# Kernel tuning notes

Hardware: AMD Instinct MI355X
Metric: run time of the kernel (lower is better)

Reference implementation:

```python
import jax, jax.numpy as jnp
import numpy as np

EPS = 1e-5


def _layer_norm(x, w, b):
    mu = jnp.mean(x, axis=-1, keepdims=True)
    var = jnp.mean(jnp.square(x - mu), axis=-1, keepdims=True)
    return (x - mu) * jax.lax.rsqrt(var + EPS) * w + b


def setup_inputs() -> dict:
    key = jax.random.key(0)
    ks = jax.random.split(key, 8)
    b, n, d, h = 1, 512, 128, 128
    edges = jax.random.normal(ks[0], (b, n, n, d), dtype=jnp.float32)
    mask = jax.random.bernoulli(ks[1], 0.9, (b, n, n))  # True = valid
    s = 0.02
    return {
        "edges": edges,
        "mask": mask,
        "ln1_w": jnp.ones((d,), jnp.float32),
        "ln1_b": jnp.zeros((d,), jnp.float32),
        "W_fg": jax.random.normal(ks[2], (4 * h, d), jnp.float32) * s,
        "b_fg": jnp.zeros((4 * h,), jnp.float32),
        "W_go": jax.random.normal(ks[3], (d, d), jnp.float32) * s,
        "b_go": jnp.zeros((d,), jnp.float32),
        "ln2_w": jnp.ones((h,), jnp.float32),
        "ln2_b": jnp.zeros((h,), jnp.float32),
        "W_out": jax.random.normal(ks[4], (d, h), jnp.float32) * s,
        "b_out": jnp.zeros((d,), jnp.float32),
    }


def reference(edges, mask, ln1_w, ln1_b, W_fg, b_fg, W_go, b_go, ln2_w, ln2_b, W_out, b_out):
    h = W_fg.shape[0] // 4
    x = _layer_norm(edges, ln1_w, ln1_b)                         # [b,n,n,d]
    fg = jnp.einsum('bijd,ed->bije', x, W_fg) + b_fg             # [b,n,n,4h]
    feats, gates = fg[..., :2 * h], fg[..., 2 * h:]
    gated = feats * jax.nn.sigmoid(gates)                        # [b,n,n,2h]
    to_feats, from_feats = gated[..., :h], gated[..., h:]
    out_gate = jax.nn.sigmoid(jnp.einsum('bijd,ed->bije', x, W_go) + b_go)
    m = mask[..., None]                                          # True = keep
    to_feats = jnp.where(m, to_feats, 0.0)
    from_feats = jnp.where(m, from_feats, 0.0)
    out_gate = jnp.where(m, out_gate, 0.0)
    # triangle outgoing: contract over shared k axis per channel d
    tri = jnp.einsum('bikd,bjkd->bijd', to_feats, from_feats)    # [b,n,n,h]
    out = jnp.einsum('bijh,dh->bijd', _layer_norm(tri, ln2_w, ln2_b), W_out) + b_out
    return out_gate * out
```

## Files before the change

kernel.cpp:

```cpp
#include <hip/hip_runtime.h>

#define NSEQ 512
#define DCH 128
#define RTOT (NSEQ * NSEQ)

typedef __attribute__((ext_vector_type(8))) short bf16x8;
typedef __attribute__((ext_vector_type(4))) float f32x4;

__device__ __forceinline__ unsigned short f2bf(float v) {
  union { float f; unsigned int u; } x; x.f = v;
  unsigned int u = x.u;
  return (unsigned short)((u + 0x7fffu + ((u >> 16) & 1u)) >> 16);
}
__device__ __forceinline__ float bf2f(unsigned short s) {
  union { unsigned int u; float f; } x; x.u = ((unsigned int)s) << 16;
  return x.f;
}
__device__ __forceinline__ float sigmoidf(float x) { return 1.f / (1.f + __expf(-x)); }

__device__ __forceinline__ void async16(const unsigned short* g, unsigned short* l) {
  __builtin_amdgcn_global_load_lds(
      (const __attribute__((address_space(1))) unsigned int*)g,
      (__attribute__((address_space(3))) unsigned int*)l, 16, 0, 0);
}

__global__ void prep_kernel(const float* __restrict__ W_fg, const float* __restrict__ b_fg,
                            const float* __restrict__ W_go, const float* __restrict__ b_go,
                            const float* __restrict__ W_out,
                            unsigned short* __restrict__ Wc, float* __restrict__ bc,
                            unsigned short* __restrict__ Woutb) {
  int idx = blockIdx.x * 256 + threadIdx.x;
  if (idx < 640 * 128) {
    int rr = idx >> 7, k = idx & 127;
    float v, bv;
    if (rr < 512) {
      int m = rr >> 7;
      int srow = (m == 1) ? rr + 128 : (m == 2) ? rr - 128 : rr;
      v = W_fg[srow * 128 + k];
      bv = b_fg[srow];
    } else {
      int srow = rr - 512;
      v = W_go[srow * 128 + k];
      bv = b_go[srow];
    }
    Wc[idx] = f2bf(v);
    if (k == 0) bc[rr] = bv;
  } else {
    int i2 = idx - 640 * 128;
    if (i2 < 128 * 128) Woutb[i2] = f2bf(W_out[i2]);
  }
}

__global__ __launch_bounds__(256) void ln1_kernel(const float* __restrict__ edges,
                                                  const float* __restrict__ w,
                                                  const float* __restrict__ b,
                                                  unsigned short* __restrict__ xb) {
  int wv = threadIdx.x >> 6;
  int lane = threadIdx.x & 63;
  size_t row = (size_t)blockIdx.x * 4 + wv;
  const float2* e = (const float2*)(edges + row * 128);
  float2 v = e[lane];
  float s = v.x + v.y, sq = v.x * v.x + v.y * v.y;
#pragma unroll
  for (int off = 32; off; off >>= 1) {
    s += __shfl_xor(s, off);
    sq += __shfl_xor(sq, off);
  }
  float mu = s * (1.f / 128.f);
  float var = sq * (1.f / 128.f) - mu * mu;
  float rs = rsqrtf(var + 1e-5f);
  int c = lane * 2;
  float x0 = (v.x - mu) * rs * w[c] + b[c];
  float x1 = (v.y - mu) * rs * w[c + 1] + b[c + 1];
  unsigned int packed = (unsigned int)f2bf(x0) | ((unsigned int)f2bf(x1) << 16);
  ((unsigned int*)(xb + row * 128))[lane] = packed;
}

__global__ __launch_bounds__(256) void fg_gemm_kernel(
    const unsigned short* __restrict__ xb, const unsigned short* __restrict__ Wc,
    const float* __restrict__ bc, const int* __restrict__ mask,
    unsigned short* __restrict__ toT, unsigned short* __restrict__ fromT) {
  __shared__ unsigned int Cs[128 * 36];
  int nb = blockIdx.y;
  int wv = threadIdx.x >> 6, lane = threadIdx.x & 63;
  int qm = lane & 15, quad = lane >> 4;
  int r0 = blockIdx.x * 64;
  int nbase = nb * 256;

  bf16x8 Bf[2][4], Bg[2][4];
#pragma unroll
  for (int ft = 0; ft < 2; ft++)
#pragma unroll
    for (int kk = 0; kk < 4; kk++) {
      int ko = kk * 32 + quad * 8;
      Bf[ft][kk] = *(const bf16x8*)(Wc + (size_t)(nbase + wv * 32 + ft * 16 + qm) * 128 + ko);
      Bg[ft][kk] = *(const bf16x8*)(Wc + (size_t)(nbase + 128 + wv * 32 + ft * 16 + qm) * 128 + ko);
    }

#pragma unroll
  for (int m = 0; m < 4; m++) {
    int rw = r0 + m * 16;
    f32x4 accf[2], accg[2];
#pragma unroll
    for (int ft = 0; ft < 2; ft++) {
      accf[ft] = (f32x4){0.f, 0.f, 0.f, 0.f};
      accg[ft] = (f32x4){0.f, 0.f, 0.f, 0.f};
    }
#pragma unroll
    for (int kk = 0; kk < 4; kk++) {
      int ko = kk * 32 + quad * 8;
      bf16x8 a = *(const bf16x8*)(xb + (size_t)(rw + qm) * 128 + ko);
#pragma unroll
      for (int ft = 0; ft < 2; ft++) {
        accf[ft] = __builtin_amdgcn_mfma_f32_16x16x32_bf16(a, Bf[ft][kk], accf[ft], 0, 0, 0);
        accg[ft] = __builtin_amdgcn_mfma_f32_16x16x32_bf16(a, Bg[ft][kk], accg[ft], 0, 0, 0);
      }
    }
    int rbase = rw + quad * 4;
    int4 mi = *(const int4*)(mask + rbase);
    float mk[4] = {mi.x ? 1.f : 0.f, mi.y ? 1.f : 0.f, mi.z ? 1.f : 0.f, mi.w ? 1.f : 0.f};
#pragma unroll
    for (int ft = 0; ft < 2; ft++) {
      int c = wv * 32 + ft * 16 + qm;
      float bF = bc[nbase + c];
      float bG = bc[nbase + 128 + c];
      float v0 = (accf[ft][0] + bF) * sigmoidf(accg[ft][0] + bG) * mk[0];
      float v1 = (accf[ft][1] + bF) * sigmoidf(accg[ft][1] + bG) * mk[1];
      float v2 = (accf[ft][2] + bF) * sigmoidf(accg[ft][2] + bG) * mk[2];
      float v3 = (accf[ft][3] + bF) * sigmoidf(accg[ft][3] + bG) * mk[3];
      unsigned int u0 = (unsigned int)f2bf(v0) | ((unsigned int)f2bf(v1) << 16);
      unsigned int u1 = (unsigned int)f2bf(v2) | ((unsigned int)f2bf(v3) << 16);
      *(uint2*)(Cs + c * 36 + m * 8 + quad * 2) = (uint2){u0, u1};
    }
  }
  __syncthreads();
  {
    unsigned short* dst = (nb == 0) ? toT : fromT;
    int pl = lane >> 3, lo = lane & 7;
#pragma unroll
    for (int i = 0; i < 4; i++) {
      int p = wv * 32 + i * 8 + pl;
      uint4 v = *(const uint4*)(Cs + p * 36 + lo * 4);
      *(uint4*)(dst + (size_t)p * RTOT + r0 + lo * 8) = v;
    }
  }
}

__global__ __launch_bounds__(256) void go_gemm_kernel(
    const unsigned short* __restrict__ xb, const unsigned short* __restrict__ Wc,
    const float* __restrict__ bc, const int* __restrict__ mask,
    float* __restrict__ gate_out) {
  int wv = threadIdx.x >> 6, lane = threadIdx.x & 63;
  int qm = lane & 15, quad = lane >> 4;
  int rw = blockIdx.x * 64 + wv * 16;

  f32x4 acc[8];
#pragma unroll
  for (int t = 0; t < 8; t++) acc[t] = (f32x4){0.f, 0.f, 0.f, 0.f};

#pragma unroll
  for (int kk = 0; kk < 4; kk++) {
    int ko = kk * 32 + quad * 8;
    bf16x8 a = *(const bf16x8*)(xb + (size_t)(rw + qm) * 128 + ko);
#pragma unroll
    for (int t = 0; t < 8; t++) {
      bf16x8 bf = *(const bf16x8*)(Wc + (size_t)(512 + t * 16 + qm) * 128 + ko);
      acc[t] = __builtin_amdgcn_mfma_f32_16x16x32_bf16(a, bf, acc[t], 0, 0, 0);
    }
  }

  int rbase = rw + quad * 4;
  int4 mi = *(const int4*)(mask + rbase);
  float mk[4] = {mi.x ? 1.f : 0.f, mi.y ? 1.f : 0.f, mi.z ? 1.f : 0.f, mi.w ? 1.f : 0.f};
#pragma unroll
  for (int t = 0; t < 8; t++) {
    int c = t * 16 + qm;
    float bG = bc[512 + c];
#pragma unroll
    for (int reg = 0; reg < 4; reg++) {
      float g = sigmoidf(acc[t][reg] + bG) * mk[reg];
      gate_out[(size_t)(rbase + reg) * 128 + c] = g;
    }
  }
}

__global__ __launch_bounds__(256) void tri_gemm_kernel(
    const unsigned short* __restrict__ toT, const unsigned short* __restrict__ fromT,
    unsigned short* __restrict__ triT) {
  __shared__ unsigned short smem[128 * 136];
  unsigned short* As = smem;
  unsigned short* Bs = smem + 128 * 64;

  int d = blockIdx.z;
  int i0 = blockIdx.x * 128, j0 = blockIdx.y * 128;
  int tid = threadIdx.x, w = tid >> 6, lane = tid & 63;
  int qm = lane & 15, quad = lane >> 4;
  int wm = w >> 1, wn = w & 1;
  const unsigned short* A = toT + (size_t)d * RTOT;
  const unsigned short* B = fromT + (size_t)d * RTOT;
  int lr = lane >> 3, lk = (lane & 7) * 8;

  f32x4 acc[4][4];
#pragma unroll
  for (int m = 0; m < 4; m++)
#pragma unroll
    for (int n = 0; n < 4; n++) acc[m][n] = (f32x4){0.f, 0.f, 0.f, 0.f};

  for (int kb = 0; kb < 512; kb += 64) {
    __syncthreads();
#pragma unroll
    for (int q = 0; q < 4; q++) {
      int blk = w * 4 + q;
      async16(A + (size_t)(i0 + blk * 8 + lr) * 512 + kb + lk, As + blk * 512);
      async16(B + (size_t)(j0 + blk * 8 + lr) * 512 + kb + lk, Bs + blk * 512);
    }
    __syncthreads();
#pragma unroll
    for (int kk = 0; kk < 2; kk++) {
      bf16x8 af[4], bfr[4];
#pragma unroll
      for (int m = 0; m < 4; m++)
        af[m] = *(const bf16x8*)(As + (wm * 64 + m * 16 + qm) * 64 + kk * 32 + quad * 8);
#pragma unroll
      for (int n = 0; n < 4; n++)
        bfr[n] = *(const bf16x8*)(Bs + (wn * 64 + n * 16 + qm) * 64 + kk * 32 + quad * 8);
#pragma unroll
      for (int m = 0; m < 4; m++)
#pragma unroll
        for (int n = 0; n < 4; n++)
          acc[m][n] = __builtin_amdgcn_mfma_f32_16x16x32_bf16(af[m], bfr[n], acc[m][n], 0, 0, 0);
    }
  }

  __syncthreads();
#pragma unroll
  for (int m = 0; m < 4; m++) {
    int rb = wm * 64 + m * 16 + quad * 4;
#pragma unroll
    for (int n = 0; n < 4; n++) {
      int col = wn * 64 + n * 16 + qm;
#pragma unroll
      for (int reg = 0; reg < 4; reg++)
        smem[(rb + reg) * 136 + col] = f2bf(acc[m][n][reg]);
    }
  }
  __syncthreads();
  {
    int row = tid >> 1, half = tid & 1;
    const uint4* src = (const uint4*)(smem + row * 136 + half * 64);
    uint4 v[8];
#pragma unroll
    for (int u = 0; u < 8; u++) v[u] = src[u];
    uint4* dst = (uint4*)(triT + (size_t)d * RTOT + (size_t)(i0 + row) * 512 + j0 + half * 64);
#pragma unroll
    for (int u = 0; u < 8; u++) dst[u] = v[u];
  }
}

__global__ __launch_bounds__(256) void out_kernel(
    const unsigned short* __restrict__ triT, const unsigned short* __restrict__ Woutb,
    const float* __restrict__ ln2w, const float* __restrict__ ln2b,
    const float* __restrict__ b_out, float* __restrict__ out,
    const unsigned short* __restrict__ xb, const unsigned short* __restrict__ Wc,
    const float* __restrict__ bc, const int* __restrict__ mask, int fuse) {
  __shared__ unsigned short nt[64][136];
  __shared__ float mu_s[64], rs_s[64];
  int r0 = blockIdx.x * 64;
  int tid = threadIdx.x;

  {
    int dch = tid >> 1, half = tid & 1;
    const uint4* src = (const uint4*)(triT + (size_t)dch * RTOT + r0 + half * 32);
    uint4 v[4];
    v[0] = src[0]; v[1] = src[1]; v[2] = src[2]; v[3] = src[3];
    const unsigned short* pv = (const unsigned short*)v;
#pragma unroll
    for (int u = 0; u < 32; u++) nt[half * 32 + u][dch] = pv[u];
  }
  __syncthreads();

  {
    int p = tid >> 2, part = tid & 3;
    float s = 0.f, sq = 0.f;
#pragma unroll
    for (int u = 0; u < 4; u++) {
      bf16x8 v = *(const bf16x8*)(&nt[p][part * 32 + u * 8]);
#pragma unroll
      for (int e = 0; e < 8; e++) {
        float f = bf2f((unsigned short)v[e]);
        s += f; sq += f * f;
      }
    }
    s += __shfl_xor(s, 1); sq += __shfl_xor(sq, 1);
    s += __shfl_xor(s, 2); sq += __shfl_xor(sq, 2);
    float mu = s * (1.f / 128.f);
    float var = sq * (1.f / 128.f) - mu * mu;
    if (part == 0) { mu_s[p] = mu; rs_s[p] = rsqrtf(var + 1e-5f); }
  }
  __syncthreads();

  int wv = tid >> 6, lane = tid & 63;
  int qm = lane & 15, quad = lane >> 4;
  int p = wv * 16 + qm;
  float mu = mu_s[p], rs = rs_s[p];

  bf16x8 afr[4];
#pragma unroll
  for (int kk = 0; kk < 4; kk++) {
    int ko = kk * 32 + quad * 8;
    bf16x8 raw = *(const bf16x8*)(&nt[p][ko]);
#pragma unroll
    for (int e = 0; e < 8; e++) {
      float wf = ln2w[ko + e], bv = ln2b[ko + e];
      afr[kk][e] = (short)f2bf((bf2f((unsigned short)raw[e]) - mu) * rs * wf + bv);
    }
  }

  f32x4 acc[8];
#pragma unroll
  for (int t = 0; t < 8; t++) acc[t] = (f32x4){0.f, 0.f, 0.f, 0.f};
#pragma unroll
  for (int kk = 0; kk < 4; kk++) {
    int ko = kk * 32 + quad * 8;
#pragma unroll
    for (int t = 0; t < 8; t++) {
      bf16x8 bf = *(const bf16x8*)(Woutb + (size_t)(t * 16 + qm) * 128 + ko);
      acc[t] = __builtin_amdgcn_mfma_f32_16x16x32_bf16(afr[kk], bf, acc[t], 0, 0, 0);
    }
  }

  int rbase = r0 + wv * 16 + quad * 4;
  if (fuse) {
    f32x4 acc2[8];
#pragma unroll
    for (int t = 0; t < 8; t++) acc2[t] = (f32x4){0.f, 0.f, 0.f, 0.f};
    const unsigned short* xrow = xb + (size_t)(r0 + wv * 16 + qm) * 128;
#pragma unroll
    for (int kk = 0; kk < 4; kk++) {
      int ko = kk * 32 + quad * 8;
      bf16x8 a2 = *(const bf16x8*)(xrow + ko);
#pragma unroll
      for (int t = 0; t < 8; t++) {
        bf16x8 bf = *(const bf16x8*)(Wc + (size_t)(512 + t * 16 + qm) * 128 + ko);
        acc2[t] = __builtin_amdgcn_mfma_f32_16x16x32_bf16(a2, bf, acc2[t], 0, 0, 0);
      }
    }
    int4 mi = *(const int4*)(mask + rbase);
    float mk[4] = {mi.x ? 1.f : 0.f, mi.y ? 1.f : 0.f, mi.z ? 1.f : 0.f, mi.w ? 1.f : 0.f};
#pragma unroll
    for (int t = 0; t < 8; t++) {
      int c = t * 16 + qm;
      float bo = b_out[c];
      float bG = bc[512 + c];
#pragma unroll
      for (int reg = 0; reg < 4; reg++) {
        float g = sigmoidf(acc2[t][reg] + bG) * mk[reg];
        out[(size_t)(rbase + reg) * 128 + c] = (acc[t][reg] + bo) * g;
      }
    }
  } else {
#pragma unroll
    for (int t = 0; t < 8; t++) {
      int c = t * 16 + qm;
      float bo = b_out[c];
#pragma unroll
      for (int reg = 0; reg < 4; reg++) {
        size_t off = (size_t)(rbase + reg) * 128 + c;
        out[off] = (acc[t][reg] + bo) * out[off];
      }
    }
  }
}

extern "C" void kernel_launch(void* const* d_in, const int* in_sizes, int n_in,
                              void* d_out, int out_size, void* d_ws, size_t ws_size,
                              hipStream_t stream) {
  const float* edges = (const float*)d_in[0];
  const int* mask = (const int*)d_in[1];
  const float* ln1w = (const float*)d_in[2];
  const float* ln1b = (const float*)d_in[3];
  const float* W_fg = (const float*)d_in[4];
  const float* b_fg = (const float*)d_in[5];
  const float* W_go = (const float*)d_in[6];
  const float* b_go = (const float*)d_in[7];
  const float* ln2w = (const float*)d_in[8];
  const float* ln2b = (const float*)d_in[9];
  const float* W_out = (const float*)d_in[10];
  const float* b_out = (const float*)d_in[11];

  char* ws = (char*)d_ws;
  const size_t SZ = (size_t)RTOT * DCH * 2;
  const size_t WSMALL = 0x40000;
  unsigned short* xb = (unsigned short*)ws;
  unsigned short* toT = (unsigned short*)(ws + SZ);
  unsigned short* fromT = (unsigned short*)(ws + 2 * SZ);
  unsigned short* Wc = (unsigned short*)(ws + 3 * SZ);
  float* bc = (float*)(ws + 3 * SZ + 640 * 128 * 2);
  unsigned short* Woutb = (unsigned short*)(ws + 3 * SZ + 640 * 128 * 2 + 640 * 4);
  float* gate = (float*)d_out;

  bool fits = ws_size >= 4 * SZ + WSMALL;
  unsigned short* triT = fits ? (unsigned short*)(ws + 3 * SZ + WSMALL) : xb;

  prep_kernel<<<384, 256, 0, stream>>>(W_fg, b_fg, W_go, b_go, W_out, Wc, bc, Woutb);
  ln1_kernel<<<RTOT / 4, 256, 0, stream>>>(edges, ln1w, ln1b, xb);
  fg_gemm_kernel<<<dim3(RTOT / 64, 2), 256, 0, stream>>>(xb, Wc, bc, mask, toT, fromT);
  if (!fits) go_gemm_kernel<<<RTOT / 64, 256, 0, stream>>>(xb, Wc, bc, mask, gate);
  tri_gemm_kernel<<<dim3(4, 4, 128), 256, 0, stream>>>(toT, fromT, triT);
  out_kernel<<<RTOT / 64, 256, 0, stream>>>(triT, Woutb, ln2w, ln2b, b_out,
                                            (float*)d_out, xb, Wc, bc, mask, fits ? 1 : 0);
}
```

Before: 625.4 us.

## Repartition output GEMM so each wave owns output columns and reuses weight fragments

```diff
diff --git a/kernel.cpp b/kernel.cpp
--- a/kernel.cpp
+++ b/kernel.cpp
@@ -301,72 +301,81 @@
 
   int wv = tid >> 6, lane = tid & 63;
   int qm = lane & 15, quad = lane >> 4;
-  int p = wv * 16 + qm;
-  float mu = mu_s[p], rs = rs_s[p];
-
-  bf16x8 afr[4];
-#pragma unroll
-  for (int kk = 0; kk < 4; kk++) {
-    int ko = kk * 32 + quad * 8;
-    bf16x8 raw = *(const bf16x8*)(&nt[p][ko]);
-#pragma unroll
-    for (int e = 0; e < 8; e++) {
-      float wf = ln2w[ko + e], bv = ln2b[ko + e];
-      afr[kk][e] = (short)f2bf((bf2f((unsigned short)raw[e]) - mu) * rs * wf + bv);
-    }
-  }
-
-  f32x4 acc[8];
-#pragma unroll
-  for (int t = 0; t < 8; t++) acc[t] = (f32x4){0.f, 0.f, 0.f, 0.f};
-#pragma unroll
-  for (int kk = 0; kk < 4; kk++) {
-    int ko = kk * 32 + quad * 8;
-#pragma unroll
-    for (int t = 0; t < 8; t++) {
-      bf16x8 bf = *(const bf16x8*)(Woutb + (size_t)(t * 16 + qm) * 128 + ko);
-      acc[t] = __builtin_amdgcn_mfma_f32_16x16x32_bf16(afr[kk], bf, acc[t], 0, 0, 0);
-    }
-  }
-
-  int rbase = r0 + wv * 16 + quad * 4;
-  if (fuse) {
-    f32x4 acc2[8];
-#pragma unroll
-    for (int t = 0; t < 8; t++) acc2[t] = (f32x4){0.f, 0.f, 0.f, 0.f};
-    const unsigned short* xrow = xb + (size_t)(r0 + wv * 16 + qm) * 128;
+
+  bf16x8 Bo[2][4], Bg[2][4];
+#pragma unroll
+  for (int ft = 0; ft < 2; ft++)
+#pragma unroll
+    for (int kk = 0; kk < 4; kk++) {
+      int c = wv * 32 + ft * 16 + qm;
+      int ko = kk * 32 + quad * 8;
+      Bo[ft][kk] = *(const bf16x8*)(Woutb + (size_t)c * 128 + ko);
+      if (fuse) Bg[ft][kk] = *(const bf16x8*)(Wc + (size_t)(512 + c) * 128 + ko);
+    }
+
+#pragma unroll
+  for (int m = 0; m < 4; m++) {
+    int rl = m * 16 + qm;
+    float mu = mu_s[rl], rs = rs_s[rl];
+
+    bf16x8 afr[4];
 #pragma unroll
     for (int kk = 0; kk < 4; kk++) {
       int ko = kk * 32 + quad * 8;
-      bf16x8 a2 = *(const bf16x8*)(xrow + ko);
-#pragma unroll
-      for (int t = 0; t < 8; t++) {
-        bf16x8 bf = *(const bf16x8*)(Wc + (size_t)(512 + t * 16 + qm) * 128 + ko);
-        acc2[t] = __builtin_amdgcn_mfma_f32_16x16x32_bf16(a2, bf, acc2[t], 0, 0, 0);
-      }
-    }
-    int4 mi = *(const int4*)(mask + rbase);
-    float mk[4] = {mi.x ? 1.f : 0.f, mi.y ? 1.f : 0.f, mi.z ? 1.f : 0.f, mi.w ? 1.f : 0.f};
-#pragma unroll
-    for (int t = 0; t < 8; t++) {
-      int c = t * 16 + qm;
-      float bo = b_out[c];
-      float bG = bc[512 + c];
-#pragma unroll
-      for (int reg = 0; reg < 4; reg++) {
-        float g = sigmoidf(acc2[t][reg] + bG) * mk[reg];
-        out[(size_t)(rbase + reg) * 128 + c] = (acc[t][reg] + bo) * g;
-      }
-    }
-  } else {
-#pragma unroll
-    for (int t = 0; t < 8; t++) {
-      int c = t * 16 + qm;
-      float bo = b_out[c];
-#pragma unroll
-      for (int reg = 0; reg < 4; reg++) {
-        size_t off = (size_t)(rbase + reg) * 128 + c;
-        out[off] = (acc[t][reg] + bo) * out[off];
+      bf16x8 raw = *(const bf16x8*)(&nt[rl][ko]);
+#pragma unroll
+      for (int e = 0; e < 8; e++) {
+        float wf = ln2w[ko + e], bv = ln2b[ko + e];
+        afr[kk][e] = (short)f2bf((bf2f((unsigned short)raw[e]) - mu) * rs * wf + bv);
+      }
+    }
+
+    f32x4 accO[2], accG[2];
+#pragma unroll
+    for (int ft = 0; ft < 2; ft++) {
+      accO[ft] = (f32x4){0.f, 0.f, 0.f, 0.f};
+      accG[ft] = (f32x4){0.f, 0.f, 0.f, 0.f};
+    }
+    const unsigned short* xrow = xb + (size_t)(r0 + rl) * 128;
+#pragma unroll
+    for (int kk = 0; kk < 4; kk++) {
+      int ko = kk * 32 + quad * 8;
+#pragma unroll
+      for (int ft = 0; ft < 2; ft++)
+        accO[ft] = __builtin_amdgcn_mfma_f32_16x16x32_bf16(afr[kk], Bo[ft][kk], accO[ft], 0, 0, 0);
+      if (fuse) {
+        bf16x8 a2 = *(const bf16x8*)(xrow + ko);
+#pragma unroll
+        for (int ft = 0; ft < 2; ft++)
+          accG[ft] = __builtin_amdgcn_mfma_f32_16x16x32_bf16(a2, Bg[ft][kk], accG[ft], 0, 0, 0);
+      }
+    }
+
+    int rbase = r0 + m * 16 + quad * 4;
+    if (fuse) {
+      int4 mi = *(const int4*)(mask + rbase);
+      float mk[4] = {mi.x ? 1.f : 0.f, mi.y ? 1.f : 0.f, mi.z ? 1.f : 0.f, mi.w ? 1.f : 0.f};
+#pragma unroll
+      for (int ft = 0; ft < 2; ft++) {
+        int c = wv * 32 + ft * 16 + qm;
+        float bo = b_out[c];
+        float bG = bc[512 + c];
+#pragma unroll
+        for (int reg = 0; reg < 4; reg++) {
+          float g = sigmoidf(accG[ft][reg] + bG) * mk[reg];
+          out[(size_t)(rbase + reg) * 128 + c] = (accO[ft][reg] + bo) * g;
+        }
+      }
+    } else {
+#pragma unroll
+      for (int ft = 0; ft < 2; ft++) {
+        int c = wv * 32 + ft * 16 + qm;
+        float bo = b_out[c];
+#pragma unroll
+        for (int reg = 0; reg < 4; reg++) {
+          size_t off = (size_t)(rbase + reg) * 128 + c;
+          out[off] = (accO[ft][reg] + bo) * out[off];
+        }
       }
     }
   }
```

Result: no change. 619.2 us (-1.0%).
